# Optimization experiments

Measured on AMD Instinct MI355X. Metric: run time of the kernel, lower is better.

Reference implementation:

```python
import jax, jax.numpy as jnp
import numpy as np

B, S, E, H, D = 4, 2048, 1024, 16, 64  # batch, seq (n_query==graph_size), embed, heads, qkv_dim


def setup_inputs() -> dict:
    key = jax.random.key(0)
    k1, k2, k3, k4, k5, k6 = jax.random.split(key, 6)
    q = jax.random.normal(k1, (B, S, E), dtype=jnp.float32)
    h = jax.random.normal(k2, (B, S, E), dtype=jnp.float32)
    # mask==True means attention NOT allowed (negative adjacency)
    mask = jax.random.randint(k3, (B, S, S), 0, 2) == 1
    scale = 0.02
    Wq = jax.random.normal(k4, (H * D, E), dtype=jnp.float32) * scale
    Wk = jax.random.normal(k5, (H * D, E), dtype=jnp.float32) * scale
    Wv = jax.random.normal(k6, (H * D, E), dtype=jnp.float32) * scale
    return {"q": q, "h": h, "mask": mask, "Wq": Wq, "Wk": Wk, "Wv": Wv}


def reference(q, h, mask, Wq, Wk, Wv):
    b, sq, e = q.shape
    sk = h.shape[1]
    hd = Wq.shape[0]
    heads = H
    d = hd // heads
    norm = 1.0 / jnp.sqrt(jnp.asarray(d, dtype=q.dtype))
    # Linear(bias=False): y = x @ W^T ; then reshape_by_heads -> (B, H, S, D)
    Q = (q @ Wq.T).reshape(b, sq, heads, d).transpose(0, 2, 1, 3)
    K = (h @ Wk.T).reshape(b, sk, heads, d).transpose(0, 2, 1, 3)
    V = (h @ Wv.T).reshape(b, sk, heads, d).transpose(0, 2, 1, 3)
    compat = norm * jnp.einsum("bhqd,bhkd->bhqk", Q, K)  # (B,H,Sq,Sk)
    compat = jnp.where(mask[:, None, :, :], -jnp.inf, compat)
    attn = jax.nn.softmax(compat, axis=-1)
    out_heads = jnp.einsum("bhqk,bhkd->bhqd", attn, V)
    # transpose(1,2) then concat heads -> (B, Sq, H*D)
    return out_heads.transpose(0, 2, 1, 3).reshape(b, sq, heads * d)
```

## Files before the change

kernel.cpp:

```cpp
#include <hip/hip_runtime.h>
#include <math.h>

#define Bb 4
#define Ss 2048
#define Ee 1024
#define Hh 16
#define Dd 64
#define HD (Hh * Dd)

typedef __attribute__((ext_vector_type(8))) _Float16 f16x8;
typedef __attribute__((ext_vector_type(4))) _Float16 f16x4;
typedef __attribute__((ext_vector_type(2))) _Float16 f16x2;
typedef __attribute__((ext_vector_type(4))) float f32x4;

__device__ __forceinline__ void gl_lds16(const void* g, void* l) {
  __builtin_amdgcn_global_load_lds(
      (const __attribute__((address_space(1))) unsigned int*)g,
      (__attribute__((address_space(3))) unsigned int*)l, 16, 0, 0);
}

__device__ __forceinline__ f16x2 pkrtz(float a, float b) {
  return __builtin_bit_cast(f16x2, __builtin_amdgcn_cvt_pkrtz(a, b));
}

#define CVT_BLOCKS 19456
__global__ __launch_bounds__(256) void prep_all(const float* __restrict__ q,
                                                const float* __restrict__ h,
                                                const float* __restrict__ wq,
                                                const float* __restrict__ wk,
                                                const float* __restrict__ wv,
                                                _Float16* __restrict__ qf,
                                                _Float16* __restrict__ hf,
                                                _Float16* __restrict__ wqf,
                                                _Float16* __restrict__ wkf,
                                                _Float16* __restrict__ wvf,
                                                const int* __restrict__ mask,
                                                unsigned long long* __restrict__ pm) {
  if (blockIdx.x < CVT_BLOCKS) {
    const int QH = (Bb * Ss * Ee) / 4;
    const int WM = (HD * Ee) / 4;
    int i = blockIdx.x * 256 + threadIdx.x;
    const float* src;
    _Float16* dst;
    int off;
    if (i < QH)                   { src = q;  dst = qf;  off = i; }
    else if (i < 2 * QH)          { src = h;  dst = hf;  off = i - QH; }
    else if (i < 2 * QH + WM)     { src = wq; dst = wqf; off = i - 2 * QH; }
    else if (i < 2 * QH + 2 * WM) { src = wk; dst = wkf; off = i - 2 * QH - WM; }
    else                          { src = wv; dst = wvf; off = i - 2 * QH - 2 * WM; }
    float4 v = ((const float4*)src)[off];
    f16x4 o;
    o.x = (_Float16)v.x; o.y = (_Float16)v.y;
    o.z = (_Float16)v.z; o.w = (_Float16)v.w;
    *(f16x4*)(dst + 4 * (size_t)off) = o;
  } else {
    const int bid = blockIdx.x - CVT_BLOCKS;
    const int wv = threadIdx.x >> 6, lane = threadIdx.x & 63;
    const size_t base = ((size_t)bid * 4 + wv) * 256;
#pragma unroll
    for (int i = 0; i < 4; ++i) {
      unsigned long long bits = __ballot(mask[base + i * 64 + lane] != 0);
      if (lane == 0) pm[(base >> 6) + i] = bits;
    }
  }
}

__global__ __launch_bounds__(512, 4) void proj_qkv(const _Float16* __restrict__ qf,
                                                   const _Float16* __restrict__ hf,
                                                   const _Float16* __restrict__ Wqf,
                                                   const _Float16* __restrict__ Wkf,
                                                   const _Float16* __restrict__ Wvf,
                                                   _Float16* __restrict__ Qb,
                                                   _Float16* __restrict__ Kb,
                                                   _Float16* __restrict__ Vb) {
  __shared__ _Float16 As[2][128 * 64];
  __shared__ _Float16 Bs[2][128 * 64];
  const int seg = blockIdx.y;
  const _Float16* A = (seg == 0) ? qf : hf;
  const _Float16* W = (seg == 0) ? Wqf : ((seg == 1) ? Wkf : Wvf);
  _Float16* Y       = (seg == 0) ? Qb  : ((seg == 1) ? Kb  : Vb);
  const float scale = (seg == 0) ? 0.18033688011112042f : 1.0f;

  const int lid = blockIdx.x;
  const int xcd = lid & 7, m = lid >> 3;
  const int stripe = xcd + 8 * (m & 3) + 32 * (m >> 5);
  const int nt = (m >> 2) & 7;
  const int bm = stripe * 128, bn = nt * 128;

  const int tid = threadIdx.x;
  const int wv = tid >> 6, lane = tid & 63;
  const int quad = lane >> 4, l16 = lane & 15;
  const int wr = wv >> 2, wc = wv & 3;

  auto stage = [&](int buf, int k0) {
#pragma unroll
    for (int i = 0; i < 2; ++i) {
      int cb = wv * 64 + i * 512;
      int c = cb + lane;
      int row = c >> 3;
      int l = (c & 7) ^ (row & 7);
      gl_lds16(A + (size_t)(bm + row) * Ee + k0 + l * 8,
               (char*)&As[buf][0] + (size_t)cb * 16);
    }
#pragma unroll
    for (int i = 0; i < 2; ++i) {
      int cb = wv * 64 + i * 512;
      int c = cb + lane;
      int row = c >> 3;
      int l = (c & 7) ^ (row & 7);
      gl_lds16(W + (size_t)(bn + row) * Ee + k0 + l * 8,
               (char*)&Bs[buf][0] + (size_t)cb * 16);
    }
  };

  f32x4 acc[4][2];
#pragma unroll
  for (int i = 0; i < 4; ++i)
#pragma unroll
    for (int j = 0; j < 2; ++j) acc[i][j] = (f32x4){0.f, 0.f, 0.f, 0.f};

  stage(0, 0);
  const int NT = Ee / 64;
  for (int it = 0; it < NT; ++it) {
    const int buf = it & 1;
    if (it + 1 < NT) {
      stage(buf ^ 1, (it + 1) * 64);
      asm volatile("s_waitcnt vmcnt(4)\n\ts_barrier" ::: "memory");
    } else {
      asm volatile("s_waitcnt vmcnt(0)\n\ts_barrier" ::: "memory");
    }
#pragma unroll
    for (int s = 0; s < 2; ++s) {
      f16x8 af[4], bf[2];
#pragma unroll
      for (int i = 0; i < 4; ++i) {
        int row = wr * 64 + i * 16 + l16;
        int l = s * 4 + quad;
        af[i] = *(const f16x8*)&As[buf][row * 64 + ((l ^ (row & 7)) << 3)];
      }
#pragma unroll
      for (int j = 0; j < 2; ++j) {
        int row = wc * 32 + j * 16 + l16;
        int l = s * 4 + quad;
        bf[j] = *(const f16x8*)&Bs[buf][row * 64 + ((l ^ (row & 7)) << 3)];
      }
#pragma unroll
      for (int i = 0; i < 4; ++i)
#pragma unroll
        for (int j = 0; j < 2; ++j)
          acc[i][j] = __builtin_amdgcn_mfma_f32_16x16x32_f16(af[i], bf[j], acc[i][j], 0, 0, 0);
    }
    asm volatile("s_barrier" ::: "memory");
  }

#pragma unroll
  for (int i = 0; i < 4; ++i)
#pragma unroll
    for (int j = 0; j < 2; ++j)
#pragma unroll
      for (int reg = 0; reg < 4; ++reg) {
        int row = bm + wr * 64 + i * 16 + quad * 4 + reg;
        int col = bn + wc * 32 + j * 16 + l16;
        Y[(size_t)row * HD + col] = (_Float16)(acc[i][j][reg] * scale);
      }
}

__global__ __launch_bounds__(256) void vtrans(const unsigned short* __restrict__ Vb,
                                              unsigned short* __restrict__ Vt) {
  __shared__ unsigned short T[64][68];
  const int nx = blockIdx.x;
  const int my = blockIdx.y;
  const int m0 = my * 64, n0 = nx * 64;
  const int bsel = m0 >> 11, s0 = m0 & 2047;
  const int tid = threadIdx.x;
  const int r = tid >> 4, c4 = (tid & 15) << 2;
#pragma unroll
  for (int i = 0; i < 4; ++i) {
    ushort4 v = *(const ushort4*)(Vb + (size_t)(m0 + r + i * 16) * HD + n0 + c4);
    T[r + i * 16][c4 + 0] = v.x; T[r + i * 16][c4 + 1] = v.y;
    T[r + i * 16][c4 + 2] = v.z; T[r + i * 16][c4 + 3] = v.w;
  }
  __syncthreads();
#pragma unroll
  for (int i = 0; i < 4; ++i) {
    ushort4 o;
    o.x = T[c4 + 0][r + i * 16]; o.y = T[c4 + 1][r + i * 16];
    o.z = T[c4 + 2][r + i * 16]; o.w = T[c4 + 3][r + i * 16];
    *(ushort4*)(Vt + ((size_t)bsel * HD + n0 + r + i * 16) * Ss + s0 + c4) = o;
  }
}

__global__ __launch_bounds__(256) void attn_mfma8(const _Float16* __restrict__ Qb,
                                                  const _Float16* __restrict__ Kb,
                                                  const _Float16* __restrict__ Vt,
                                                  const unsigned long long* __restrict__ pm,
                                                  float* __restrict__ out) {
  const int gid = blockIdx.x;
  const int xcd = gid & 7, m = gid >> 3;
  const int bq = m & 15;
  const int p  = xcd + 8 * (m >> 4);
  const int h  = p & 15;
  const int b  = p >> 4;
  const int tid  = threadIdx.x;
  const int wv   = tid >> 6;
  const int lane = tid & 63;
  const int quad = lane >> 4;
  const int l16  = lane & 15;

  __shared__ _Float16 Ks[64][64];
  __shared__ _Float16 Vs[64][64];

  const int q0g = bq * 128 + wv * 32;
  f16x8 qf[2][2];
#pragma unroll
  for (int g = 0; g < 2; ++g) {
    const _Float16* qrow = Qb + ((size_t)b * Ss + q0g + g * 16 + l16) * HD + h * Dd;
    qf[g][0] = *(const f16x8*)(qrow + quad * 8);
    qf[g][1] = *(const f16x8*)(qrow + 32 + quad * 8);
  }

  const int r = tid >> 2, c = (tid & 3) << 4;
  const int swzr = (r & 7) ^ ((r & 4) >> 2);
  const int pw0 = ((c >> 3) ^ swzr) << 3;
  const int pw1 = pw0 ^ 8;
  const int swzl = (l16 & 7) ^ ((l16 & 4) >> 2);

  const _Float16* kbase = Kb + ((size_t)b * Ss + r) * HD + h * Dd + c;
  const _Float16* vbase = Vt + (((size_t)b * Hh + h) * Dd + r) * Ss + c;

  const unsigned long long* pmrow0 = pm + ((size_t)b * Ss + q0g + l16) * (Ss >> 6);
  const size_t pmg = (size_t)16 * (Ss >> 6);

  f32x4 O[2][4];
#pragma unroll
  for (int g = 0; g < 2; ++g)
#pragma unroll
    for (int dt = 0; dt < 4; ++dt) O[g][dt] = (f32x4){0.f, 0.f, 0.f, 0.f};
  float lsum[2] = {0.f, 0.f};
  const f16x2 one2 = {(_Float16)1.0f, (_Float16)1.0f};
  const f32x4 zero4 = (f32x4){0.f, 0.f, 0.f, 0.f};

  f16x8 ka = *(const f16x8*)kbase;
  f16x8 kb2 = *(const f16x8*)(kbase + 8);
  f16x8 va = *(const f16x8*)vbase;
  f16x8 vb2 = *(const f16x8*)(vbase + 8);
  unsigned long long mqn0 = ~pmrow0[0];
  unsigned long long mqn1 = ~pmrow0[pmg];

  for (int kt = 0; kt < Ss; kt += 64) {
    asm volatile("s_waitcnt lgkmcnt(0)\n\ts_barrier" ::: "memory");
    *(f16x8*)&Ks[r][pw0] = ka;
    *(f16x8*)&Ks[r][pw1] = kb2;
    *(f16x8*)&Vs[r][pw0] = va;
    *(f16x8*)&Vs[r][pw1] = vb2;
    const unsigned long long mq0 = mqn0, mq1 = mqn1;
    {
      const int ktn = (kt + 64) & (Ss - 1);
      ka  = *(const f16x8*)(kbase + (size_t)ktn * HD);
      kb2 = *(const f16x8*)(kbase + (size_t)ktn * HD + 8);
      va  = *(const f16x8*)(vbase + ktn);
      vb2 = *(const f16x8*)(vbase + ktn + 8);
      const int itn = (ktn >> 6);
      mqn0 = ~pmrow0[itn];
      mqn1 = ~pmrow0[pmg + itn];
    }
    asm volatile("s_waitcnt lgkmcnt(0)\n\ts_barrier" ::: "memory");

    f32x4 c4[2][4];
    __builtin_amdgcn_s_setprio(1);
#pragma unroll
    for (int sub = 0; sub < 4; ++sub) {
      const _Float16* krow = &Ks[sub * 16 + l16][0];
      const int off0 = (quad ^ swzl) << 3;
      f16x8 k0 = *(const f16x8*)(krow + off0);
      f16x8 k1 = *(const f16x8*)(krow + (off0 ^ 32));
#pragma unroll
      for (int g = 0; g < 2; ++g) {
        c4[g][sub] = __builtin_amdgcn_mfma_f32_16x16x32_f16(k0, qf[g][0], zero4, 0, 0, 0);
        c4[g][sub] = __builtin_amdgcn_mfma_f32_16x16x32_f16(k1, qf[g][1], c4[g][sub], 0, 0, 0);
      }
    }
    __builtin_amdgcn_s_setprio(0);

    f16x4 pf[2][4];
#pragma unroll
    for (int g = 0; g < 2; ++g) {
      const unsigned long long mqs = (g ? mq1 : mq0) >> (quad * 4);
      const unsigned kw0 = (unsigned)mqs;
      const unsigned kw1 = (unsigned)(mqs >> 32);
#pragma unroll
      for (int sub = 0; sub < 4; ++sub) {
        const unsigned word = (sub < 2) ? kw0 : kw1;
        float p[4];
#pragma unroll
        for (int reg = 0; reg < 4; ++reg) {
          const int pos = (sub & 1) * 16 + reg;
          const unsigned keep = (unsigned)(((int)(word << (31 - pos))) >> 31);
          float e = __builtin_amdgcn_exp2f(c4[g][sub][reg]);
          p[reg] = __builtin_bit_cast(float,
                     __builtin_bit_cast(unsigned, e) & keep);
        }
        f16x2 lo = pkrtz(p[0], p[1]);
        f16x2 hi = pkrtz(p[2], p[3]);
#if __has_builtin(__builtin_amdgcn_fdot2)
        lsum[g] = __builtin_amdgcn_fdot2(lo, one2, lsum[g], false);
        lsum[g] = __builtin_amdgcn_fdot2(hi, one2, lsum[g], false);
#else
        lsum[g] += (p[0] + p[1]) + (p[2] + p[3]);
#endif
        pf[g][sub] = __builtin_shufflevector(lo, hi, 0, 1, 2, 3);
      }
    }

    __builtin_amdgcn_s_setprio(1);
#pragma unroll
    for (int dt = 0; dt < 4; ++dt) {
      const _Float16* vrow = &Vs[dt * 16 + l16][0];
#pragma unroll
      for (int sub = 0; sub < 4; ++sub) {
        f16x4 vf = *(const f16x4*)(vrow + ((((2 * sub + (quad >> 1)) ^ swzl) << 3) +
                                           ((quad & 1) << 2)));
#pragma unroll
        for (int g = 0; g < 2; ++g)
          O[g][dt] = __builtin_amdgcn_mfma_f32_16x16x16f16(vf, pf[g][sub], O[g][dt], 0, 0, 0);
      }
    }
    __builtin_amdgcn_s_setprio(0);
  }

#pragma unroll
  for (int g = 0; g < 2; ++g) {
    float ls = lsum[g];
    ls += __shfl_xor(ls, 16, 64);
    ls += __shfl_xor(ls, 32, 64);
    const float inv = 1.0f / ls;
    float* obase = out + ((size_t)b * Ss + q0g + g * 16 + l16) * HD + h * Dd;
#pragma unroll
    for (int dt = 0; dt < 4; ++dt) {
      float4 st;
      st.x = O[g][dt][0] * inv; st.y = O[g][dt][1] * inv;
      st.z = O[g][dt][2] * inv; st.w = O[g][dt][3] * inv;
      *(float4*)(obase + dt * 16 + quad * 4) = st;
    }
  }
}

extern "C" void kernel_launch(void* const* d_in, const int* in_sizes, int n_in,
                              void* d_out, int out_size, void* d_ws, size_t ws_size,
                              hipStream_t stream) {
  const float* q    = (const float*)d_in[0];
  const float* h    = (const float*)d_in[1];
  const int*   mask = (const int*)d_in[2];
  const float* Wq   = (const float*)d_in[3];
  const float* Wk   = (const float*)d_in[4];
  const float* Wv   = (const float*)d_in[5];
  float* out = (float*)d_out;

  char* ws = (char*)d_ws;
  const size_t MB = 1024 * 1024;
  _Float16* qf  = (_Float16*)(ws);
  _Float16* hf  = (_Float16*)(ws + 16 * MB);
  _Float16* Wqf = (_Float16*)(ws + 32 * MB);
  _Float16* Wkf = (_Float16*)(ws + 34 * MB);
  _Float16* Wvf = (_Float16*)(ws + 36 * MB);
  _Float16* Qb  = (_Float16*)(ws + 38 * MB);
  _Float16* Kb  = (_Float16*)(ws + 54 * MB);
  _Float16* Vb  = (_Float16*)(ws + 70 * MB);
  _Float16* Vt  = (_Float16*)(ws);
  unsigned long long* pm = (unsigned long long*)(ws + 86 * MB);

  const int mask_blocks = (Bb * Ss * Ss) / 1024;
  prep_all<<<CVT_BLOCKS + mask_blocks, 256, 0, stream>>>(
      q, h, Wq, Wk, Wv, qf, hf, Wqf, Wkf, Wvf, mask, pm);

  proj_qkv<<<dim3(512, 3), 512, 0, stream>>>(qf, hf, Wqf, Wkf, Wvf, Qb, Kb, Vb);

  vtrans<<<dim3(HD / 64, (Bb * Ss) / 64), 256, 0, stream>>>((const unsigned short*)Vb,
                                                            (unsigned short*)Vt);

  attn_mfma8<<<1024, 256, 0, stream>>>(Qb, Kb, Vt, pm, out);
}
```

Measured before the change: 354.8 us.

## Fuse V transpose into projection epilogue and use 4-wave 64x64 warp tiles

The projection GEMM now writes V directly in transposed (B, HD, S) layout from its accumulators, which removes the separate vtrans kernel and its extra read and write of the full V tensor. The block also drops from 8 waves to 4, with each wave computing a 64x64 tile (16 accumulators), and the block-to-tile mapping is simplified. This raises per-wave register pressure and lowers the number of waves per block, which may reduce latency hiding. The transposed stores are 4-element vectors strided by Ss and less coalesced than row stores.

```diff
diff --git a/kernel.cpp b/kernel.cpp
--- a/kernel.cpp
+++ b/kernel.cpp
@@ -65,37 +65,36 @@
   }
 }
 
-__global__ __launch_bounds__(512, 4) void proj_qkv(const _Float16* __restrict__ qf,
-                                                   const _Float16* __restrict__ hf,
-                                                   const _Float16* __restrict__ Wqf,
-                                                   const _Float16* __restrict__ Wkf,
-                                                   const _Float16* __restrict__ Wvf,
-                                                   _Float16* __restrict__ Qb,
-                                                   _Float16* __restrict__ Kb,
-                                                   _Float16* __restrict__ Vb) {
+__global__ __launch_bounds__(256) void proj_qkv(const _Float16* __restrict__ qf,
+                                                const _Float16* __restrict__ hf,
+                                                const _Float16* __restrict__ Wqf,
+                                                const _Float16* __restrict__ Wkf,
+                                                const _Float16* __restrict__ Wvf,
+                                                _Float16* __restrict__ Qb,
+                                                _Float16* __restrict__ Kb,
+                                                _Float16* __restrict__ Vt) {
   __shared__ _Float16 As[2][128 * 64];
   __shared__ _Float16 Bs[2][128 * 64];
   const int seg = blockIdx.y;
   const _Float16* A = (seg == 0) ? qf : hf;
   const _Float16* W = (seg == 0) ? Wqf : ((seg == 1) ? Wkf : Wvf);
-  _Float16* Y       = (seg == 0) ? Qb  : ((seg == 1) ? Kb  : Vb);
   const float scale = (seg == 0) ? 0.18033688011112042f : 1.0f;
 
   const int lid = blockIdx.x;
   const int xcd = lid & 7, m = lid >> 3;
-  const int stripe = xcd + 8 * (m & 3) + 32 * (m >> 5);
-  const int nt = (m >> 2) & 7;
+  const int stripe = xcd + 8 * (m >> 3);
+  const int nt = m & 7;
   const int bm = stripe * 128, bn = nt * 128;
 
   const int tid = threadIdx.x;
   const int wv = tid >> 6, lane = tid & 63;
   const int quad = lane >> 4, l16 = lane & 15;
-  const int wr = wv >> 2, wc = wv & 3;
+  const int wr = wv >> 1, wc = wv & 1;
 
   auto stage = [&](int buf, int k0) {
 #pragma unroll
-    for (int i = 0; i < 2; ++i) {
-      int cb = wv * 64 + i * 512;
+    for (int i = 0; i < 4; ++i) {
+      int cb = wv * 64 + i * 256;
       int c = cb + lane;
       int row = c >> 3;
       int l = (c & 7) ^ (row & 7);
@@ -103,8 +102,8 @@
                (char*)&As[buf][0] + (size_t)cb * 16);
     }
 #pragma unroll
-    for (int i = 0; i < 2; ++i) {
-      int cb = wv * 64 + i * 512;
+    for (int i = 0; i < 4; ++i) {
+      int cb = wv * 64 + i * 256;
       int c = cb + lane;
       int row = c >> 3;
       int l = (c & 7) ^ (row & 7);
@@ -113,11 +112,11 @@
     }
   };
 
-  f32x4 acc[4][2];
+  f32x4 acc[4][4];
 #pragma unroll
   for (int i = 0; i < 4; ++i)
 #pragma unroll
-    for (int j = 0; j < 2; ++j) acc[i][j] = (f32x4){0.f, 0.f, 0.f, 0.f};
+    for (int j = 0; j < 4; ++j) acc[i][j] = (f32x4){0.f, 0.f, 0.f, 0.f};
 
   stage(0, 0);
   const int NT = Ee / 64;
@@ -125,13 +124,13 @@
     const int buf = it & 1;
     if (it + 1 < NT) {
       stage(buf ^ 1, (it + 1) * 64);
-      asm volatile("s_waitcnt vmcnt(4)\n\ts_barrier" ::: "memory");
+      asm volatile("s_waitcnt vmcnt(8)\n\ts_barrier" ::: "memory");
     } else {
       asm volatile("s_waitcnt vmcnt(0)\n\ts_barrier" ::: "memory");
     }
 #pragma unroll
     for (int s = 0; s < 2; ++s) {
-      f16x8 af[4], bf[2];
+      f16x8 af[4], bf[4];
 #pragma unroll
       for (int i = 0; i < 4; ++i) {
         int row = wr * 64 + i * 16 + l16;
@@ -139,54 +138,46 @@
         af[i] = *(const f16x8*)&As[buf][row * 64 + ((l ^ (row & 7)) << 3)];
       }
 #pragma unroll
-      for (int j = 0; j < 2; ++j) {
-        int row = wc * 32 + j * 16 + l16;
+      for (int j = 0; j < 4; ++j) {
+        int row = wc * 64 + j * 16 + l16;
         int l = s * 4 + quad;
         bf[j] = *(const f16x8*)&Bs[buf][row * 64 + ((l ^ (row & 7)) << 3)];
       }
 #pragma unroll
       for (int i = 0; i < 4; ++i)
 #pragma unroll
-        for (int j = 0; j < 2; ++j)
+        for (int j = 0; j < 4; ++j)
           acc[i][j] = __builtin_amdgcn_mfma_f32_16x16x32_f16(af[i], bf[j], acc[i][j], 0, 0, 0);
     }
     asm volatile("s_barrier" ::: "memory");
   }
 
-#pragma unroll
-  for (int i = 0; i < 4; ++i)
-#pragma unroll
-    for (int j = 0; j < 2; ++j)
-#pragma unroll
-      for (int reg = 0; reg < 4; ++reg) {
-        int row = bm + wr * 64 + i * 16 + quad * 4 + reg;
-        int col = bn + wc * 32 + j * 16 + l16;
-        Y[(size_t)row * HD + col] = (_Float16)(acc[i][j][reg] * scale);
-      }
-}
-
-__global__ __launch_bounds__(256) void vtrans(const unsigned short* __restrict__ Vb,
-                                              unsigned short* __restrict__ Vt) {
-  __shared__ unsigned short T[64][68];
-  const int nx = blockIdx.x;
-  const int my = blockIdx.y;
-  const int m0 = my * 64, n0 = nx * 64;
-  const int bsel = m0 >> 11, s0 = m0 & 2047;
-  const int tid = threadIdx.x;
-  const int r = tid >> 4, c4 = (tid & 15) << 2;
-#pragma unroll
-  for (int i = 0; i < 4; ++i) {
-    ushort4 v = *(const ushort4*)(Vb + (size_t)(m0 + r + i * 16) * HD + n0 + c4);
-    T[r + i * 16][c4 + 0] = v.x; T[r + i * 16][c4 + 1] = v.y;
-    T[r + i * 16][c4 + 2] = v.z; T[r + i * 16][c4 + 3] = v.w;
-  }
-  __syncthreads();
-#pragma unroll
-  for (int i = 0; i < 4; ++i) {
-    ushort4 o;
-    o.x = T[c4 + 0][r + i * 16]; o.y = T[c4 + 1][r + i * 16];
-    o.z = T[c4 + 2][r + i * 16]; o.w = T[c4 + 3][r + i * 16];
-    *(ushort4*)(Vt + ((size_t)bsel * HD + n0 + r + i * 16) * Ss + s0 + c4) = o;
+  if (seg < 2) {
+    _Float16* Y = (seg == 0) ? Qb : Kb;
+#pragma unroll
+    for (int i = 0; i < 4; ++i)
+#pragma unroll
+      for (int j = 0; j < 4; ++j)
+#pragma unroll
+        for (int reg = 0; reg < 4; ++reg) {
+          int row = bm + wr * 64 + i * 16 + quad * 4 + reg;
+          int col = bn + wc * 64 + j * 16 + l16;
+          Y[(size_t)row * HD + col] = (_Float16)(acc[i][j][reg] * scale);
+        }
+  } else {
+    const int bvt = bm >> 11;
+    const int sbase = (bm & 2047) + wr * 64;
+#pragma unroll
+    for (int i = 0; i < 4; ++i)
+#pragma unroll
+      for (int j = 0; j < 4; ++j) {
+        const int s0 = sbase + i * 16 + quad * 4;
+        const int col = bn + wc * 64 + j * 16 + l16;
+        f16x2 lo = pkrtz(acc[i][j][0], acc[i][j][1]);
+        f16x2 hi = pkrtz(acc[i][j][2], acc[i][j][3]);
+        f16x4 val = __builtin_shufflevector(lo, hi, 0, 1, 2, 3);
+        *(f16x4*)(Vt + ((size_t)bvt * HD + col) * Ss + s0) = val;
+      }
   }
 }
 
@@ -365,18 +356,14 @@
   _Float16* Wvf = (_Float16*)(ws + 36 * MB);
   _Float16* Qb  = (_Float16*)(ws + 38 * MB);
   _Float16* Kb  = (_Float16*)(ws + 54 * MB);
-  _Float16* Vb  = (_Float16*)(ws + 70 * MB);
-  _Float16* Vt  = (_Float16*)(ws);
+  _Float16* Vt  = (_Float16*)(ws + 70 * MB);
   unsigned long long* pm = (unsigned long long*)(ws + 86 * MB);
 
   const int mask_blocks = (Bb * Ss * Ss) / 1024;
   prep_all<<<CVT_BLOCKS + mask_blocks, 256, 0, stream>>>(
       q, h, Wq, Wk, Wv, qf, hf, Wqf, Wkf, Wvf, mask, pm);
 
-  proj_qkv<<<dim3(512, 3), 512, 0, stream>>>(qf, hf, Wqf, Wkf, Wvf, Qb, Kb, Vb);
-
-  vtrans<<<dim3(HD / 64, (Bb * Ss) / 64), 256, 0, stream>>>((const unsigned short*)Vb,
-                                                            (unsigned short*)Vt);
+  proj_qkv<<<dim3(512, 3), 256, 0, stream>>>(qf, hf, Wqf, Wkf, Wvf, Qb, Kb, Vt);
 
   attn_mfma8<<<1024, 256, 0, stream>>>(Qb, Kb, Vt, pm, out);
 }
```

Measured after the change: 352.5 us. No clear change (-0.6%).
